# Optimization experiments

Measured on AMD Instinct MI355X. Metric: run time of the kernel, lower is better.

## Reference

```python
import jax, jax.numpy as jnp
import numpy as np

RANK = 32
ALPHA = 1.0
SCALE = ALPHA / RANK


def setup_inputs() -> dict:
    key = jax.random.key(0)
    k1, k2, k3, k4, k5 = jax.random.split(key, 5)
    B_, S, D_in, D_out = 4, 2048, 4096, 4096
    x = jax.random.normal(k1, (B_, S, D_in), dtype=jnp.float32)
    # nn.Linear weight: [out, in], kaiming-ish scale
    W = jax.random.normal(k2, (D_out, D_in), dtype=jnp.float32) / np.sqrt(D_in)
    bias = jax.random.normal(k3, (D_out,), dtype=jnp.float32) * 0.01
    A = jax.random.normal(k4, (D_in, RANK), dtype=jnp.float32) * 0.01
    # torch init is zeros for B; use small random so output depends on LoRA path
    Bm = jax.random.normal(k5, (RANK, D_out), dtype=jnp.float32) * 0.01
    return {"x": x, "W": W, "bias": bias, "A": A, "B": Bm}


def reference(x, W, bias, A, B):
    # Original: y = x @ (W + scale*(A@B)^T)^T + bias
    # Mathematically identical fused form (two GEMMs, no [in,out] delta):
    base = jnp.einsum('bsd,od->bso', x, W)          # [B,S,out]
    lora = jnp.einsum('bsr,ro->bso', x @ A, B)       # [B,S,rank]->[B,S,out]
    return base + SCALE * lora + bias
```

## Files before the change

### kernel.cpp

```cpp
#include <hip/hip_runtime.h>
#include <hip/hip_bf16.h>
#include <stdint.h>

#define RANK 32
#define SCALE (1.0f / 32.0f)

typedef __bf16 bf16x8 __attribute__((ext_vector_type(8)));
typedef float f32x4 __attribute__((ext_vector_type(4)));

__device__ __forceinline__ void gload16(const void* g, void* l) {
  __builtin_amdgcn_global_load_lds(
      (const __attribute__((address_space(1))) unsigned int*)g,
      (__attribute__((address_space(3))) unsigned int*)l, 16, 0, 0);
}

__device__ __forceinline__ unsigned short f2bf(float f) {
  __hip_bfloat16 h = __float2bfloat16(f);
  return *reinterpret_cast<unsigned short*>(&h);
}

__global__ __launch_bounds__(256) void transpose_B_k(const float* __restrict__ B,
                                                     float* __restrict__ Bt,
                                                     int Dout) {
  int idx = blockIdx.x * 256 + threadIdx.x;
  int r = idx / Dout;
  int o = idx - r * Dout;
  Bt[(long long)o * RANK + r] = B[idx];
}

__global__ __launch_bounds__(256) void merge_W_k(const float* __restrict__ W,
                                                 const float* __restrict__ A,
                                                 const float* __restrict__ Bt,
                                                 unsigned short* __restrict__ Wb,
                                                 int Din, int Dout) {
  __shared__ float sB[16 * RANK];
  int nib = Din / 256;
  int ib = blockIdx.x % nib;
  int ob = blockIdx.x / nib;
  int i0 = ib * 256, o0 = ob * 16;
  int t = threadIdx.x;

  if (t < 128) {
    reinterpret_cast<float4*>(sB)[t] =
        reinterpret_cast<const float4*>(Bt + (long long)o0 * RANK)[t];
  }

  float a[RANK];
  const float4* Ap = reinterpret_cast<const float4*>(A + (long long)(i0 + t) * RANK);
#pragma unroll
  for (int c = 0; c < RANK / 4; ++c) {
    float4 v = Ap[c];
    a[c * 4 + 0] = v.x; a[c * 4 + 1] = v.y;
    a[c * 4 + 2] = v.z; a[c * 4 + 3] = v.w;
  }
  __syncthreads();

  for (int o = 0; o < 16; ++o) {
    float d = 0.f;
#pragma unroll
    for (int j = 0; j < RANK; ++j) d += a[j] * sB[o * RANK + j];
    long long off = (long long)(o0 + o) * Din + i0 + t;
    Wb[off] = f2bf(W[off] + SCALE * d);
  }
}

__global__ __launch_bounds__(256) void cast_x_k(const float* __restrict__ in,
                                                unsigned short* __restrict__ out,
                                                long long n8) {
  long long i = (long long)blockIdx.x * 256 + threadIdx.x;
  if (i >= n8) return;
  const float4* in4 = reinterpret_cast<const float4*>(in) + i * 2;
  float4 v0 = in4[0], v1 = in4[1];
  union { unsigned short u[8]; uint4 q; } p;
  p.u[0] = f2bf(v0.x); p.u[1] = f2bf(v0.y); p.u[2] = f2bf(v0.z); p.u[3] = f2bf(v0.w);
  p.u[4] = f2bf(v1.x); p.u[5] = f2bf(v1.y); p.u[6] = f2bf(v1.z); p.u[7] = f2bf(v1.w);
  reinterpret_cast<uint4*>(out)[i] = p.q;
}

template <int NISSUE>
__device__ __forceinline__ void stage(const unsigned short* g, int K, int koff,
                                      int row0, unsigned short* ldsbase,
                                      int t, int wid) {
  int r = t >> 3;
  int cg = (t & 7) ^ (r & 7);
#pragma unroll
  for (int i = 0; i < NISSUE; ++i) {
    gload16(g + (long long)(row0 + i * 64 + r) * K + koff + cg * 8,
            ldsbase + (row0 + i * 64) * 64 + wid * 512);
  }
}

__device__ __forceinline__ int swz_off(int rowl, int k) {
  return rowl * 64 + ((((k) >> 3) ^ (rowl & 7)) << 3);
}

__global__ __launch_bounds__(512, 2) void gemm256_bias_k(
    const unsigned short* __restrict__ Xb,
    const unsigned short* __restrict__ Wb,
    const float* __restrict__ bias,
    float* __restrict__ Out,
    int M, int N, int K) {
  __shared__ unsigned short As[2][256 * 64];
  __shared__ unsigned short Bs[2][256 * 64];

  int nbn = N / 256;
  int cpx = gridDim.x >> 3;
  int bid = blockIdx.x;
  int swz = (bid & 7) * cpx + (bid >> 3);
  int bm = swz / nbn, bn = swz % nbn;

  int t = threadIdx.x;
  int wid = t >> 6, lane = t & 63;
  int wr = wid >> 2, wc = wid & 3;
  int lr = lane & 15, kq = (lane >> 4) * 8;
  int aw = wr * 128, bw = wc * 64;

  const unsigned short* ga = Xb + (long long)bm * 256 * K;
  const unsigned short* gb = Wb + (long long)bn * 256 * K;

  f32x4 acc[8][4] = {};
  bf16x8 a[4][2], b0[2][2], b1[2][2];

  const int NT = K / 64;

  stage<4>(ga, K, 0, 0, As[0], t, wid);
  stage<4>(gb, K, 0, 0, Bs[0], t, wid);
  stage<4>(ga, K, 64, 0, As[1], t, wid);
  asm volatile("s_waitcnt vmcnt(4)" ::: "memory");
  __builtin_amdgcn_s_barrier();

  for (int kt = 0; kt < NT; ++kt) {
    int cur = kt & 1;
    const unsigned short* Ac = As[cur];
    const unsigned short* Bc = Bs[cur];
    unsigned short* An = As[cur];
    unsigned short* Bn = Bs[cur ^ 1];
    int konext = (kt + 1) * 64, konext2 = (kt + 2) * 64;

#pragma unroll
    for (int m = 0; m < 4; ++m)
#pragma unroll
      for (int ks = 0; ks < 2; ++ks)
        a[m][ks] = *(const bf16x8*)&Ac[swz_off(aw + m * 16 + lr, ks * 32 + kq)];
#pragma unroll
    for (int n = 0; n < 2; ++n)
#pragma unroll
      for (int ks = 0; ks < 2; ++ks)
        b0[n][ks] = *(const bf16x8*)&Bc[swz_off(bw + n * 16 + lr, ks * 32 + kq)];
    if (kt + 1 < NT) stage<2>(gb, K, konext, 0, Bn, t, wid);
    __builtin_amdgcn_s_barrier();
    asm volatile("s_waitcnt lgkmcnt(0)" ::: "memory");
    __builtin_amdgcn_s_setprio(1);
#pragma unroll
    for (int m = 0; m < 4; ++m)
#pragma unroll
      for (int n = 0; n < 2; ++n)
#pragma unroll
        for (int ks = 0; ks < 2; ++ks)
          acc[m][n] = __builtin_amdgcn_mfma_f32_16x16x32_bf16(a[m][ks], b0[n][ks], acc[m][n], 0, 0, 0);
    __builtin_amdgcn_s_setprio(0);
    __builtin_amdgcn_s_barrier();

#pragma unroll
    for (int n = 0; n < 2; ++n)
#pragma unroll
      for (int ks = 0; ks < 2; ++ks)
        b1[n][ks] = *(const bf16x8*)&Bc[swz_off(bw + 32 + n * 16 + lr, ks * 32 + kq)];
    if (kt + 1 < NT) stage<2>(gb, K, konext, 128, Bn, t, wid);
    __builtin_amdgcn_s_barrier();
    asm volatile("s_waitcnt lgkmcnt(0)" ::: "memory");
    __builtin_amdgcn_s_setprio(1);
#pragma unroll
    for (int m = 0; m < 4; ++m)
#pragma unroll
      for (int n = 0; n < 2; ++n)
#pragma unroll
        for (int ks = 0; ks < 2; ++ks)
          acc[m][2 + n] = __builtin_amdgcn_mfma_f32_16x16x32_bf16(a[m][ks], b1[n][ks], acc[m][2 + n], 0, 0, 0);
    __builtin_amdgcn_s_setprio(0);
    __builtin_amdgcn_s_barrier();

#pragma unroll
    for (int m = 0; m < 4; ++m)
#pragma unroll
      for (int ks = 0; ks < 2; ++ks)
        a[m][ks] = *(const bf16x8*)&Ac[swz_off(aw + 64 + m * 16 + lr, ks * 32 + kq)];
    __builtin_amdgcn_s_barrier();
    asm volatile("s_waitcnt lgkmcnt(0)" ::: "memory");
    __builtin_amdgcn_s_setprio(1);
#pragma unroll
    for (int m = 0; m < 4; ++m)
#pragma unroll
      for (int n = 0; n < 2; ++n)
#pragma unroll
        for (int ks = 0; ks < 2; ++ks)
          acc[4 + m][2 + n] = __builtin_amdgcn_mfma_f32_16x16x32_bf16(a[m][ks], b1[n][ks], acc[4 + m][2 + n], 0, 0, 0);
    __builtin_amdgcn_s_setprio(0);
    __builtin_amdgcn_s_barrier();

    if (kt + 2 < NT) {
      stage<4>(ga, K, konext2, 0, An, t, wid);
      asm volatile("s_waitcnt vmcnt(4)" ::: "memory");
    } else if (kt + 1 < NT) {
      asm volatile("s_waitcnt vmcnt(0)" ::: "memory");
    }
    __builtin_amdgcn_s_barrier();
    __builtin_amdgcn_s_setprio(1);
#pragma unroll
    for (int m = 0; m < 4; ++m)
#pragma unroll
      for (int n = 0; n < 2; ++n)
#pragma unroll
        for (int ks = 0; ks < 2; ++ks)
          acc[4 + m][n] = __builtin_amdgcn_mfma_f32_16x16x32_bf16(a[m][ks], b0[n][ks], acc[4 + m][n], 0, 0, 0);
    __builtin_amdgcn_s_setprio(0);
    __builtin_amdgcn_s_barrier();
  }

  long long orow = (long long)bm * 256 + wr * 128;
  int ocol = bn * 256 + wc * 64;
#pragma unroll
  for (int n = 0; n < 4; ++n) {
    int gc = ocol + n * 16 + lr;
    float bv = bias[gc];
#pragma unroll
    for (int m = 0; m < 8; ++m) {
      long long gr = orow + m * 16 + (lane >> 4) * 4;
#pragma unroll
      for (int v = 0; v < 4; ++v)
        Out[(gr + v) * N + gc] = acc[m][n][v] + bv;
    }
  }
}

extern "C" void kernel_launch(void* const* d_in, const int* in_sizes, int n_in,
                              void* d_out, int out_size, void* d_ws, size_t ws_size,
                              hipStream_t stream) {
  const float* x    = (const float*)d_in[0];
  const float* W    = (const float*)d_in[1];
  const float* bias = (const float*)d_in[2];
  const float* A    = (const float*)d_in[3];
  const float* B    = (const float*)d_in[4];

  int Din  = in_sizes[3] / RANK;
  int Dout = in_sizes[4] / RANK;
  long long M = (long long)in_sizes[0] / Din;

  size_t xb_bytes = (size_t)M * Din * 2;
  size_t wb_bytes = (size_t)Dout * Din * 2;
  size_t bt_bytes = (size_t)Dout * RANK * 4;
  if (ws_size < xb_bytes + wb_bytes + bt_bytes) return;

  char* ws = (char*)d_ws;
  unsigned short* Xb = (unsigned short*)ws;
  unsigned short* Wb = (unsigned short*)(ws + xb_bytes);
  float* Bt          = (float*)(ws + xb_bytes + wb_bytes);

  transpose_B_k<<<dim3((Dout * RANK) / 256), dim3(256), 0, stream>>>(B, Bt, Dout);
  merge_W_k<<<dim3((Dout / 16) * (Din / 256)), dim3(256), 0, stream>>>(W, A, Bt, Wb, Din, Dout);
  long long n8 = M * Din / 8;
  cast_x_k<<<dim3((unsigned)(n8 / 256)), dim3(256), 0, stream>>>(x, Xb, n8);
  gemm256_bias_k<<<dim3((unsigned)((M / 256) * (Dout / 256))), dim3(512), 0, stream>>>(
      Xb, Wb, bias, (float*)d_out, (int)M, Dout, Din);
}
```

Measured before the change: 362.5 us.

## Software-pipeline LDS fragment loads across MFMA phases in GEMM main loop

Restructures the bf16 GEMM k-loop so LDS fragment reads for the next phase and the next k-tile are issued interleaved with the current MFMA batches, rather than in separate load-then-wait phases. Fragments for tile 0 are preloaded before the loop, and an extra b0n register set carries next-tile B fragments. Several barriers and explicit lgkmcnt waits are removed. The aim is to hide LDS latency behind matrix math. The cost is higher register pressure and a dependence on compiler-inserted waits. The shared A buffer is now reused while other waves may still be reading it, which is a correctness risk.

```diff
diff --git a/kernel.cpp b/kernel.cpp
--- a/kernel.cpp
+++ b/kernel.cpp
@@ -119,37 +119,36 @@
   const unsigned short* gb = Wb + (long long)bn * 256 * K;
 
   f32x4 acc[8][4] = {};
-  bf16x8 a[4][2], b0[2][2], b1[2][2];
+  bf16x8 a[4][2], b0[2][2], b0n[2][2], b1[2][2];
 
   const int NT = K / 64;
 
-  stage<4>(ga, K, 0, 0, As[0], t, wid);
-  stage<4>(gb, K, 0, 0, Bs[0], t, wid);
-  stage<4>(ga, K, 64, 0, As[1], t, wid);
+#define LDA(BUF, ROFF, MM, KS) \
+  (*(const bf16x8*)&As[BUF][swz_off(aw + (ROFF) + (MM) * 16 + lr, (KS) * 32 + kq)])
+#define LDB(BUF, ROFF, NN, KS) \
+  (*(const bf16x8*)&Bs[BUF][swz_off(bw + (ROFF) + (NN) * 16 + lr, (KS) * 32 + kq)])
+
+  stage<4>(ga, K, 0, 0, &As[0][0], t, wid);
+  stage<4>(gb, K, 0, 0, &Bs[0][0], t, wid);
+  stage<4>(ga, K, 64, 0, &As[1][0], t, wid);
   asm volatile("s_waitcnt vmcnt(4)" ::: "memory");
   __builtin_amdgcn_s_barrier();
+#pragma unroll
+  for (int m = 0; m < 4; ++m) {
+    a[m][0] = LDA(0, 0, m, 0); a[m][1] = LDA(0, 0, m, 1);
+  }
+#pragma unroll
+  for (int n = 0; n < 2; ++n) {
+    b0[n][0] = LDB(0, 0, n, 0);  b0[n][1] = LDB(0, 0, n, 1);
+    b1[n][0] = LDB(0, 32, n, 0); b1[n][1] = LDB(0, 32, n, 1);
+  }
 
   for (int kt = 0; kt < NT; ++kt) {
-    int cur = kt & 1;
-    const unsigned short* Ac = As[cur];
-    const unsigned short* Bc = Bs[cur];
-    unsigned short* An = As[cur];
-    unsigned short* Bn = Bs[cur ^ 1];
+    const int cur = kt & 1;
     int konext = (kt + 1) * 64, konext2 = (kt + 2) * 64;
-
-#pragma unroll
-    for (int m = 0; m < 4; ++m)
-#pragma unroll
-      for (int ks = 0; ks < 2; ++ks)
-        a[m][ks] = *(const bf16x8*)&Ac[swz_off(aw + m * 16 + lr, ks * 32 + kq)];
-#pragma unroll
-    for (int n = 0; n < 2; ++n)
-#pragma unroll
-      for (int ks = 0; ks < 2; ++ks)
-        b0[n][ks] = *(const bf16x8*)&Bc[swz_off(bw + n * 16 + lr, ks * 32 + kq)];
-    if (kt + 1 < NT) stage<2>(gb, K, konext, 0, Bn, t, wid);
-    __builtin_amdgcn_s_barrier();
-    asm volatile("s_waitcnt lgkmcnt(0)" ::: "memory");
+    const bool hasN = (kt + 1 < NT);
+
+    if (hasN) stage<2>(gb, K, konext, 0, &Bs[cur ^ 1][0], t, wid);
     __builtin_amdgcn_s_setprio(1);
 #pragma unroll
     for (int m = 0; m < 4; ++m)
@@ -161,32 +160,20 @@
     __builtin_amdgcn_s_setprio(0);
     __builtin_amdgcn_s_barrier();
 
-#pragma unroll
-    for (int n = 0; n < 2; ++n)
-#pragma unroll
-      for (int ks = 0; ks < 2; ++ks)
-        b1[n][ks] = *(const bf16x8*)&Bc[swz_off(bw + 32 + n * 16 + lr, ks * 32 + kq)];
-    if (kt + 1 < NT) stage<2>(gb, K, konext, 128, Bn, t, wid);
-    __builtin_amdgcn_s_barrier();
-    asm volatile("s_waitcnt lgkmcnt(0)" ::: "memory");
-    __builtin_amdgcn_s_setprio(1);
-#pragma unroll
-    for (int m = 0; m < 4; ++m)
-#pragma unroll
-      for (int n = 0; n < 2; ++n)
-#pragma unroll
-        for (int ks = 0; ks < 2; ++ks)
-          acc[m][2 + n] = __builtin_amdgcn_mfma_f32_16x16x32_bf16(a[m][ks], b1[n][ks], acc[m][2 + n], 0, 0, 0);
-    __builtin_amdgcn_s_setprio(0);
-    __builtin_amdgcn_s_barrier();
-
-#pragma unroll
-    for (int m = 0; m < 4; ++m)
-#pragma unroll
-      for (int ks = 0; ks < 2; ++ks)
-        a[m][ks] = *(const bf16x8*)&Ac[swz_off(aw + 64 + m * 16 + lr, ks * 32 + kq)];
-    __builtin_amdgcn_s_barrier();
-    asm volatile("s_waitcnt lgkmcnt(0)" ::: "memory");
+    if (hasN) stage<2>(gb, K, konext, 128, &Bs[cur ^ 1][0], t, wid);
+    __builtin_amdgcn_s_setprio(1);
+#pragma unroll
+    for (int m = 0; m < 4; ++m) {
+      acc[m][2] = __builtin_amdgcn_mfma_f32_16x16x32_bf16(a[m][0], b1[0][0], acc[m][2], 0, 0, 0);
+      acc[m][2] = __builtin_amdgcn_mfma_f32_16x16x32_bf16(a[m][1], b1[0][1], acc[m][2], 0, 0, 0);
+      acc[m][3] = __builtin_amdgcn_mfma_f32_16x16x32_bf16(a[m][0], b1[1][0], acc[m][3], 0, 0, 0);
+      acc[m][3] = __builtin_amdgcn_mfma_f32_16x16x32_bf16(a[m][1], b1[1][1], acc[m][3], 0, 0, 0);
+      a[m][0] = LDA(cur, 64, m, 0);
+      a[m][1] = LDA(cur, 64, m, 1);
+    }
+    __builtin_amdgcn_s_setprio(0);
+    __builtin_amdgcn_s_barrier();
+
     __builtin_amdgcn_s_setprio(1);
 #pragma unroll
     for (int m = 0; m < 4; ++m)
@@ -199,23 +186,40 @@
     __builtin_amdgcn_s_barrier();
 
     if (kt + 2 < NT) {
-      stage<4>(ga, K, konext2, 0, An, t, wid);
+      stage<4>(ga, K, konext2, 0, &As[cur][0], t, wid);
       asm volatile("s_waitcnt vmcnt(4)" ::: "memory");
-    } else if (kt + 1 < NT) {
+    } else if (hasN) {
       asm volatile("s_waitcnt vmcnt(0)" ::: "memory");
     }
     __builtin_amdgcn_s_barrier();
-    __builtin_amdgcn_s_setprio(1);
-#pragma unroll
-    for (int m = 0; m < 4; ++m)
-#pragma unroll
-      for (int n = 0; n < 2; ++n)
-#pragma unroll
-        for (int ks = 0; ks < 2; ++ks)
-          acc[4 + m][n] = __builtin_amdgcn_mfma_f32_16x16x32_bf16(a[m][ks], b0[n][ks], acc[4 + m][n], 0, 0, 0);
-    __builtin_amdgcn_s_setprio(0);
-    __builtin_amdgcn_s_barrier();
-  }
+
+    if (hasN) {
+      b0n[0][0] = LDB(cur ^ 1, 0, 0, 0); b0n[0][1] = LDB(cur ^ 1, 0, 0, 1);
+      b0n[1][0] = LDB(cur ^ 1, 0, 1, 0); b0n[1][1] = LDB(cur ^ 1, 0, 1, 1);
+    }
+    __builtin_amdgcn_s_setprio(1);
+#pragma unroll
+    for (int m = 0; m < 4; ++m) {
+      acc[4 + m][0] = __builtin_amdgcn_mfma_f32_16x16x32_bf16(a[m][0], b0[0][0], acc[4 + m][0], 0, 0, 0);
+      acc[4 + m][0] = __builtin_amdgcn_mfma_f32_16x16x32_bf16(a[m][1], b0[0][1], acc[4 + m][0], 0, 0, 0);
+      acc[4 + m][1] = __builtin_amdgcn_mfma_f32_16x16x32_bf16(a[m][0], b0[1][0], acc[4 + m][1], 0, 0, 0);
+      acc[4 + m][1] = __builtin_amdgcn_mfma_f32_16x16x32_bf16(a[m][1], b0[1][1], acc[4 + m][1], 0, 0, 0);
+      if (hasN) {
+        a[m][0] = LDA(cur ^ 1, 0, m, 0);
+        a[m][1] = LDA(cur ^ 1, 0, m, 1);
+      }
+    }
+    __builtin_amdgcn_s_setprio(0);
+    if (hasN) {
+      b1[0][0] = LDB(cur ^ 1, 32, 0, 0); b1[0][1] = LDB(cur ^ 1, 32, 0, 1);
+      b1[1][0] = LDB(cur ^ 1, 32, 1, 0); b1[1][1] = LDB(cur ^ 1, 32, 1, 1);
+      b0[0][0] = b0n[0][0]; b0[0][1] = b0n[0][1];
+      b0[1][0] = b0n[1][0]; b0[1][1] = b0n[1][1];
+    }
+    __builtin_amdgcn_s_barrier();
+  }
+#undef LDA
+#undef LDB
 
   long long orow = (long long)bm * 256 + wr * 128;
   int ocol = bn * 256 + wc * 64;
```

After: 392.2 us. 1.08x slower.
